# Performance work log

Hardware: AMD Instinct MI355X
Metric: run time of the kernel (lower is better)

The kernel has to match this reference:

```python
import jax, jax.numpy as jnp
import numpy as np

ST_HIDDEN = 128
ST_HEADS = 4
ST_LAYERS = 3
RES_SCALE = 1.0
DK = ST_HIDDEN // ST_HEADS


def build_3d_adj(spatial_ei, spatial_ea, n_nodes, window):
    # replicate spatial edges per time slice with node offset t*n_nodes
    offs = (jnp.arange(window) * n_nodes)[None, :, None]  # [1,W,1]
    all_sp_idx = (spatial_ei[:, None, :] + offs).reshape(2, -1)  # [2, W*E]
    all_sp_attr = jnp.tile(spatial_ea, (window, 1))  # [W*E, De]
    # temporal edges t -> t+1 for every node
    src = jnp.arange((window - 1) * n_nodes)
    temp_idx = jnp.stack([src, src + n_nodes], axis=0)  # [2, (W-1)*N]
    temp_attr = jnp.broadcast_to(spatial_ea.mean(axis=0, keepdims=True),
                                 (temp_idx.shape[1], spatial_ea.shape[1]))
    ei = jnp.concatenate([all_sp_idx, temp_idx], axis=1)
    ea = jnp.concatenate([all_sp_attr, temp_attr], axis=0)
    return ei, ea


def seg_softmax(logits, dst, num_nodes):
    # logits [E,H], segment softmax over dst (pyg_softmax)
    m = jax.ops.segment_max(logits, dst, num_segments=num_nodes)  # [N,H]
    ex = jnp.exp(logits - m[dst])
    s = jax.ops.segment_sum(ex, dst, num_segments=num_nodes)
    return ex / (s[dst] + 1e-16)


def layernorm(x, g, b, eps=1e-5):
    mu = x.mean(-1, keepdims=True)
    var = ((x - mu) ** 2).mean(-1, keepdims=True)
    return (x - mu) * jax.lax.rsqrt(var + eps) * g + b


def block(x, ei, ea, qw, qb, kw, kb, vw, vb, fw, fb, ow, ob, ln_g, ln_b):
    B, Nt, _ = x.shape
    H, dk = ST_HEADS, DK
    Q = (x @ qw + qb).reshape(B, Nt, H, dk)
    K = (x @ kw + kb).reshape(B, Nt, H, dk)
    V = (x @ vw + vb).reshape(B, Nt, H, dk)
    src, dst = ei[0], ei[1]
    q_e = Q[:, dst]  # [B,E,H,dk]
    k_e = K[:, src]
    v_e = V[:, src]
    film = ea @ fw + fb  # [E, 2*hidden]
    gamma, beta = jnp.split(film, 2, axis=-1)
    gamma = gamma.reshape(1, -1, H, dk)
    beta = beta.reshape(1, -1, H, dk)
    k_e = k_e * (1.0 + gamma) + beta
    logits = (q_e * k_e).sum(-1) / np.sqrt(dk).astype(np.float32)  # [B,E,H]
    att = jax.vmap(lambda l: seg_softmax(l, dst, Nt))(logits)
    msg = att[..., None] * v_e  # [B,E,H,dk]
    out = jnp.zeros((B, Nt, H, dk), x.dtype).at[:, dst].add(msg)
    y = out.reshape(B, Nt, H * dk) @ ow + ob
    return layernorm(x + y, ln_g, ln_b)


def setup_inputs() -> dict:
    key = jax.random.key(0)
    ks = jax.random.split(key, 12)
    B, W, N, Fin, E, De = 2, 16, 1000, 16, 16000, 8
    H, L = ST_HIDDEN, ST_LAYERS
    g = lambda k, s: jax.random.normal(k, s, jnp.float32) * 0.05
    return {
        "xw": jax.random.normal(ks[0], (B, W, N, Fin), jnp.float32),
        "spatial_ei": jax.random.randint(ks[1], (2, E), 0, N),
        "spatial_ea": jax.random.normal(ks[2], (E, De), jnp.float32),
        "in_w": g(ks[3], (Fin, H)), "in_b": jnp.zeros((H,), jnp.float32),
        "qw": g(ks[4], (L, H, H)), "qb": jnp.zeros((L, H), jnp.float32),
        "kw": g(ks[5], (L, H, H)), "kb": jnp.zeros((L, H), jnp.float32),
        "vw": g(ks[6], (L, H, H)), "vb": jnp.zeros((L, H), jnp.float32),
        "fw": g(ks[7], (L, De, 2 * H)), "fb": jnp.zeros((L, 2 * H), jnp.float32),
        "ow": g(ks[8], (L, H, H)), "ob": jnp.zeros((L, H), jnp.float32),
        "ln_g": jnp.ones((L, H), jnp.float32), "ln_b": jnp.zeros((L, H), jnp.float32),
        "head_w": g(ks[9], (H, 1)), "head_b": jnp.zeros((1,), jnp.float32),
    }


def reference(xw, spatial_ei, spatial_ea, in_w, in_b, qw, qb, kw, kb, vw, vb,
              fw, fb, ow, ob, ln_g, ln_b, head_w, head_b):
    B, W, N, Fin = xw.shape
    ei, ea = build_3d_adj(spatial_ei, spatial_ea, N, W)
    x = xw.reshape(B, W * N, Fin) @ in_w + in_b
    for l in range(ST_LAYERS):
        bx = block(x, ei, ea, qw[l], qb[l], kw[l], kb[l], vw[l], vb[l],
                   fw[l], fb[l], ow[l], ob[l], ln_g[l], ln_b[l])
        x = x + RES_SCALE * (bx - x)
    last = x.reshape(B, W, N, -1)[:, -1]  # [B,N,H]
    return jax.nn.softplus(last @ head_w + head_b).squeeze(-1)  # [B,N]
```

## Files before the change

kernel.cpp:

```cpp
#include <hip/hip_runtime.h>
#include <math.h>

constexpr int B    = 2;
constexpr int W    = 16;
constexpr int N    = 1000;
constexpr int FIN  = 16;
constexpr int E    = 16000;
constexpr int DE   = 8;
constexpr int H    = 128;
constexpr int L    = 3;
constexpr int WL   = 4;
constexpr int W0G  = 12;
constexpr int RPB  = WL * N;
constexpr int ROWS = B * RPB;

__device__ __forceinline__ float blockSum128(float v) {
  #pragma unroll
  for (int off = 32; off >= 1; off >>= 1) v += __shfl_xor(v, off);
  __shared__ float s2[2];
  int w = threadIdx.x >> 6;
  __syncthreads();
  if ((threadIdx.x & 63) == 0) s2[w] = v;
  __syncthreads();
  return s2[0] + s2[1];
}

__global__ void k_count_scan(const int* __restrict__ ei, int* __restrict__ offs,
                             int* __restrict__ cursor, float* __restrict__ meanea) {
  __shared__ int cnt[N];
  __shared__ int scn[1024];
  int t = threadIdx.x;
  if (t < 8) meanea[t] = 0.f;
  if (t < N) cnt[t] = 0;
  __syncthreads();
  int vals[16];
  int nv = 0;
  for (int e = t; e < E; e += 1024) vals[nv++] = ei[E + e];
  for (int i = 0; i < nv; i++) atomicAdd(&cnt[vals[i]], 1);
  __syncthreads();
  int v = (t < N) ? cnt[t] : 0;
  scn[t] = v;
  __syncthreads();
  for (int st = 1; st < 1024; st <<= 1) {
    int add = (t >= st) ? scn[t - st] : 0;
    __syncthreads();
    scn[t] += add;
    __syncthreads();
  }
  if (t < N) {
    offs[t + 1] = scn[t];
    if (t == 0) offs[0] = 0;
    cursor[t] = scn[t] - v;
  }
}

__global__ void k_prep2(const int* __restrict__ ei, const float* __restrict__ ea,
                        int* __restrict__ cursor, int* __restrict__ csr_src,
                        int* __restrict__ csr_eid, float* __restrict__ meanea) {
  int bid = blockIdx.x;
  int t = threadIdx.x;
  if (bid < 64) {
    int e = bid * 256 + t;
    if (e < E) {
      int src = ei[e];
      int dst = ei[E + e];
      int pos = atomicAdd(&cursor[dst], 1);
      csr_src[pos] = src;
      csr_eid[pos] = e;
    }
  } else {
    __shared__ float sbuf[256];
    int d = t & 7, g = t >> 3;
    float s = 0.f;
    for (int e = (bid - 64) * 32 + g; e < E; e += 64 * 32) s += ea[e * DE + d];
    sbuf[t] = s;
    __syncthreads();
    for (int st = 16; st >= 1; st >>= 1) {
      if (g < st) sbuf[g * 8 + d] += sbuf[(g + st) * 8 + d];
      __syncthreads();
    }
    if (g == 0) atomicAdd(&meanea[d], sbuf[d]);
  }
}

__global__ void k_gemm(const float* __restrict__ X, const float* __restrict__ xw,
                       const float* __restrict__ in_w, const float* __restrict__ in_b,
                       const float* __restrict__ Wq, const float* __restrict__ bq,
                       const float* __restrict__ Wk, const float* __restrict__ bk,
                       const float* __restrict__ Wv, const float* __restrict__ bv,
                       float* __restrict__ Cq, float* __restrict__ Ck, float* __restrict__ Cv,
                       float* __restrict__ xout,
                       int base, int tpb, int fuse_in) {
  int m = blockIdx.y;
  const float* Wm = (m == 0) ? Wq : (m == 1) ? Wk : Wv;
  const float* bm = (m == 0) ? bq : (m == 1) ? bk : bv;
  float* Cm       = (m == 0) ? Cq : (m == 1) ? Ck : Cv;
  int bb = blockIdx.x / tpb;
  int t  = blockIdx.x % tpb;
  int lr0 = base + t * 16;
  int tid = threadIdx.x;
  __shared__ float xs[16][H];
  if (fuse_in) {
    __shared__ float xws[16][FIN];
    for (int i = tid; i < 16 * FIN; i += 128) {
      int rr = i >> 4, k = i & 15;
      int lr = lr0 + rr;
      if (lr < RPB) {
        int wl = lr / N, n = lr % N;
        xws[rr][k] = xw[(((long)bb * W + (W0G + wl)) * N + n) * FIN + k];
      }
    }
    __syncthreads();
    float bc = in_b[tid];
    #pragma unroll
    for (int rr = 0; rr < 16; rr++) {
      float acc = bc;
      #pragma unroll
      for (int k = 0; k < FIN; k++) acc += xws[rr][k] * in_w[k * H + tid];
      xs[rr][tid] = acc;
      int lr = lr0 + rr;
      if (m == 0 && lr < RPB) xout[((long)bb * RPB + lr) * H + tid] = acc;
    }
  } else {
    #pragma unroll
    for (int rr = 0; rr < 16; rr++) {
      int lr = lr0 + rr;
      if (lr < RPB) xs[rr][tid] = X[((long)bb * RPB + lr) * H + tid];
    }
  }
  __syncthreads();
  float bc = bm[tid];
  float acc[16];
  #pragma unroll
  for (int r = 0; r < 16; r++) acc[r] = bc;
  #pragma unroll 4
  for (int k = 0; k < H; k++) {
    float w = Wm[k * H + tid];
    #pragma unroll
    for (int r = 0; r < 16; r++) acc[r] += xs[r][k] * w;
  }
  #pragma unroll
  for (int r = 0; r < 16; r++) {
    int lr = lr0 + r;
    if (lr < RPB) Cm[((long)bb * RPB + lr) * H + tid] = acc[r];
  }
}

__global__ void k_attn_oln(const float* __restrict__ Qb, const float* __restrict__ Kb,
                           const float* __restrict__ Vb,
                           const float* __restrict__ ea, const float* __restrict__ meanea,
                           const float* __restrict__ fw, const float* __restrict__ fb,
                           const int* __restrict__ offs, const int* __restrict__ csr_src,
                           const int* __restrict__ csr_eid,
                           const float* __restrict__ x, const float* __restrict__ ow,
                           const float* __restrict__ ob, const float* __restrict__ lng,
                           const float* __restrict__ lnb, float* __restrict__ xo,
                           int out_lo,
                           const float* __restrict__ hw, const float* __restrict__ hb,
                           float* __restrict__ out, int do_head) {
  __shared__ float fwS[DE][2 * H];
  int tid = threadIdx.x;
  for (int i = tid; i < DE * 2 * H; i += H) fwS[i >> 8][i & 255] = fw[i];

  int nwin = WL - out_lo;
  int idx = blockIdx.x;
  int b = idx / (nwin * N);
  int rem = idx % (nwin * N);
  int wl = out_lo + rem / N;
  int n = rem % N;
  long drow = ((long)b * WL + wl) * N + n;
  float q = Qb[drow * H + tid];
  float fbg = fb[tid], fbb = fb[H + tid];
  long sbase = ((long)b * WL + wl) * N;
  long trow  = ((long)b * WL + wl - 1) * N + n;
  const float scale = 0.17677669529663687f;
  int i0 = offs[n], i1 = offs[n + 1];
  __syncthreads();

  float m = -INFINITY, ssum = 0.f, acc = 0.f;
  for (int base = i0; base <= i1; base += 4) {
    float l[4], vv[4];
    #pragma unroll
    for (int j = 0; j < 4; j++) {
      int i = base + j;
      if (i > i1) { l[j] = -INFINITY; vv[j] = 0.f; continue; }
      long srow; const float* eap; float esc;
      if (i < i1) { srow = sbase + csr_src[i]; eap = ea + (long)csr_eid[i] * DE; esc = 1.f; }
      else        { srow = trow;               eap = meanea;                    esc = 1.f / E; }
      float kv = Kb[srow * H + tid];
      vv[j]    = Vb[srow * H + tid];
      float4 a0 = *(const float4*)(eap);
      float4 a1 = *(const float4*)(eap + 4);
      float a[DE] = {a0.x * esc, a0.y * esc, a0.z * esc, a0.w * esc,
                     a1.x * esc, a1.y * esc, a1.z * esc, a1.w * esc};
      float g = fbg, be = fbb;
      #pragma unroll
      for (int d = 0; d < DE; d++) {
        g  += a[d] * fwS[d][tid];
        be += a[d] * fwS[d][H + tid];
      }
      float p = q * (kv * (1.f + g) + be);
      p += __shfl_xor(p, 16);
      p += __shfl_xor(p, 8);
      p += __shfl_xor(p, 4);
      p += __shfl_xor(p, 2);
      p += __shfl_xor(p, 1);
      l[j] = p * scale;
    }
    float mn = m;
    #pragma unroll
    for (int j = 0; j < 4; j++) mn = fmaxf(mn, l[j]);
    float sc  = __expf(m - mn);
    float pe0 = __expf(l[0] - mn);
    float pe1 = __expf(l[1] - mn);
    float pe2 = __expf(l[2] - mn);
    float pe3 = __expf(l[3] - mn);
    ssum = ssum * sc + ((pe0 + pe1) + (pe2 + pe3));
    acc  = acc  * sc + ((pe0 * vv[0] + pe1 * vv[1]) + (pe2 * vv[2] + pe3 * vv[3]));
    m = mn;
  }
  float ab = acc / (ssum + 1e-16f);

  __shared__ float sab[H];
  sab[tid] = ab;
  __syncthreads();
  float y = ob[tid];
  #pragma unroll 8
  for (int k = 0; k < H; k++) y += sab[k] * ow[k * H + tid];

  float v = x[drow * H + tid] + y;
  float mu = blockSum128(v) * (1.f / H);
  float dv = v - mu;
  float var = blockSum128(dv * dv) * (1.f / H);
  float o = dv * rsqrtf(var + 1e-5f) * lng[tid] + lnb[tid];

  if (!do_head) {
    xo[drow * H + tid] = o;
  } else {
    float hv = o * hw[tid];
    float tot = blockSum128(hv);
    if (tid == 0) {
      float z = tot + hb[0];
      out[b * N + n] = fmaxf(z, 0.f) + log1pf(expf(-fabsf(z)));
    }
  }
}

extern "C" void kernel_launch(void* const* d_in, const int* in_sizes, int n_in,
                              void* d_out, int out_size, void* d_ws, size_t ws_size,
                              hipStream_t stream) {
  const float* xw   = (const float*)d_in[0];
  const int*   ei   = (const int*)d_in[1];
  const float* ea   = (const float*)d_in[2];
  const float* in_w = (const float*)d_in[3];
  const float* in_b = (const float*)d_in[4];
  const float* qw   = (const float*)d_in[5];
  const float* qb   = (const float*)d_in[6];
  const float* kw   = (const float*)d_in[7];
  const float* kb   = (const float*)d_in[8];
  const float* vw   = (const float*)d_in[9];
  const float* vb   = (const float*)d_in[10];
  const float* fw   = (const float*)d_in[11];
  const float* fb   = (const float*)d_in[12];
  const float* ow   = (const float*)d_in[13];
  const float* ob   = (const float*)d_in[14];
  const float* ln_g = (const float*)d_in[15];
  const float* ln_b = (const float*)d_in[16];
  const float* hw   = (const float*)d_in[17];
  const float* hb   = (const float*)d_in[18];
  float* out = (float*)d_out;

  float* ws   = (float*)d_ws;
  float* x    = ws;
  float* x2   = x  + (long)ROWS * H;
  float* Qb   = x2 + (long)ROWS * H;
  float* Kb   = Qb + (long)ROWS * H;
  float* Vb   = Kb + (long)ROWS * H;
  float* meanea  = Vb + (long)ROWS * H;
  int* offs    = (int*)(meanea + 8);
  int* cursor  = offs + N + 1;
  int* csr_src = cursor + N;
  int* csr_eid = csr_src + E;

  k_count_scan<<<1, 1024, 0, stream>>>(ei, offs, cursor, meanea);
  k_prep2<<<128, 256, 0, stream>>>(ei, ea, cursor, csr_src, csr_eid, meanea);

  float* xa = x;
  float* xb = x2;
  for (int l = 0; l < L; l++) {
    int in_lo = l, out_lo = l + 1;
    int rows_pb = (WL - in_lo) * N;
    int tpb = (rows_pb + 15) / 16;
    k_gemm<<<dim3(B * tpb, 3), H, 0, stream>>>(
        xa, xw, in_w, in_b,
        qw + (long)l * H * H, qb + (long)l * H, kw + (long)l * H * H, kb + (long)l * H,
        vw + (long)l * H * H, vb + (long)l * H, Qb, Kb, Vb, xa,
        in_lo * N, tpb, (l == 0) ? 1 : 0);
    int nout = B * (WL - out_lo) * N;
    int last = (l == L - 1) ? 1 : 0;
    k_attn_oln<<<nout, H, 0, stream>>>(
        Qb, Kb, Vb, ea, meanea,
        fw + (long)l * DE * 2 * H, fb + (long)l * 2 * H,
        offs, csr_src, csr_eid,
        xa, ow + (long)l * H * H, ob + (long)l * H,
        ln_g + (long)l * H, ln_b + (long)l * H, xb, out_lo,
        hw, hb, out, last);
    float* tmp = xa; xa = xb; xb = tmp;
  }
}
```

Baseline: 288.8 us.

## Pre-pack weights as float4, retile QKV GEMM, move input projection into prep

Adds a prep stage that repacks all Q/K/V/O weight matrices into a k-grouped float4 layout and computes the input projection there rather than inside the first GEMM. The QKV GEMM now uses 256-thread blocks over 64-row tiles, with each thread holding an 8x4 output register tile and reading weights and activations as float4. The attention kernel keeps the FiLM weights in registers instead of shared memory, drops a barrier, uses DPP for the first two lanes of the head reduction, and reads the packed output weights as float4. The intent is fewer memory transactions and more reuse of each load in the GEMM, at the cost of extra workspace, a larger prep kernel and higher register pressure.

```diff
diff --git a/kernel.cpp b/kernel.cpp
--- a/kernel.cpp
+++ b/kernel.cpp
@@ -13,6 +13,7 @@
 constexpr int W0G  = 12;
 constexpr int RPB  = WL * N;
 constexpr int ROWS = B * RPB;
+constexpr int NMAT = 12;
 
 __device__ __forceinline__ float blockSum128(float v) {
   #pragma unroll
@@ -23,6 +24,26 @@
   if ((threadIdx.x & 63) == 0) s2[w] = v;
   __syncthreads();
   return s2[0] + s2[1];
+}
+
+__device__ __forceinline__ float dpp_add_xor1(float x) {
+  int y = __builtin_amdgcn_update_dpp(0, __float_as_int(x), 0xB1, 0xF, 0xF, true);
+  return x + __int_as_float(y);
+}
+__device__ __forceinline__ float dpp_add_xor2(float x) {
+  int y = __builtin_amdgcn_update_dpp(0, __float_as_int(x), 0x4E, 0xF, 0xF, true);
+  return x + __int_as_float(y);
+}
+__device__ __forceinline__ float headSum32(float p) {
+  p = dpp_add_xor1(p);
+  p = dpp_add_xor2(p);
+  p += __shfl_xor(p, 4);
+  p += __shfl_xor(p, 8);
+  p += __shfl_xor(p, 16);
+  return p;
+}
+__device__ __forceinline__ float dot4(float4 a, float4 b) {
+  return a.x * b.x + a.y * b.y + a.z * b.z + a.w * b.w;
 }
 
 __global__ void k_count_scan(const int* __restrict__ ei, int* __restrict__ offs,
@@ -56,7 +77,12 @@
 
 __global__ void k_prep2(const int* __restrict__ ei, const float* __restrict__ ea,
                         int* __restrict__ cursor, int* __restrict__ csr_src,
-                        int* __restrict__ csr_eid, float* __restrict__ meanea) {
+                        int* __restrict__ csr_eid, float* __restrict__ meanea,
+                        const float* __restrict__ qw, const float* __restrict__ kw,
+                        const float* __restrict__ vw, const float* __restrict__ ow,
+                        float4* __restrict__ wTp4,
+                        const float* __restrict__ xw, const float* __restrict__ in_w,
+                        const float* __restrict__ in_b, float* __restrict__ x) {
   int bid = blockIdx.x;
   int t = threadIdx.x;
   if (bid < 64) {
@@ -68,7 +94,7 @@
       csr_src[pos] = src;
       csr_eid[pos] = e;
     }
-  } else {
+  } else if (bid < 128) {
     __shared__ float sbuf[256];
     int d = t & 7, g = t >> 3;
     float s = 0.f;
@@ -80,69 +106,105 @@
       __syncthreads();
     }
     if (g == 0) atomicAdd(&meanea[d], sbuf[d]);
-  }
-}
-
-__global__ void k_gemm(const float* __restrict__ X, const float* __restrict__ xw,
-                       const float* __restrict__ in_w, const float* __restrict__ in_b,
-                       const float* __restrict__ Wq, const float* __restrict__ bq,
-                       const float* __restrict__ Wk, const float* __restrict__ bk,
-                       const float* __restrict__ Wv, const float* __restrict__ bv,
+  } else if (bid < 128 + NMAT * 16) {
+    int bid2 = bid - 128;
+    int mat = bid2 / 16;
+    int pair = bid2 % 16;
+    int kk4 = pair * 2 + (t >> 7);
+    int c = t & 127;
+    int l = mat >> 2, mm = mat & 3;
+    const float* src = ((mm == 0) ? qw : (mm == 1) ? kw : (mm == 2) ? vw : ow) + (long)l * H * H;
+    int k0 = kk4 * 4;
+    float4 v4;
+    v4.x = src[(k0 + 0) * H + c];
+    v4.y = src[(k0 + 1) * H + c];
+    v4.z = src[(k0 + 2) * H + c];
+    v4.w = src[(k0 + 3) * H + c];
+    wTp4[((long)mat * 32 + kk4) * H + c] = v4;
+  } else {
+    int bi = bid - (128 + NMAT * 16);
+    int b = bi / 63, tt = bi % 63;
+    int lr0 = tt * 64;
+    __shared__ float xwS[64][FIN];
+    __shared__ float inS[FIN][H];
+    for (int i = t; i < 64 * FIN; i += 256) {
+      int r = i >> 4, k = i & 15;
+      int lr = lr0 + r;
+      float val = 0.f;
+      if (lr < RPB) {
+        int wl = lr / N, n = lr % N;
+        val = xw[(((long)b * W + (W0G + wl)) * N + n) * FIN + k];
+      }
+      xwS[r][k] = val;
+    }
+    for (int i = t; i < FIN * H; i += 256) inS[i >> 7][i & 127] = in_w[i];
+    __syncthreads();
+    #pragma unroll
+    for (int qi = 0; qi < 8; qi++) {
+      int idx = t + qi * 256;
+      int r = idx >> 5, cq = idx & 31;
+      int lr = lr0 + r;
+      if (lr < RPB) {
+        float4 acc = *(const float4*)(in_b + cq * 4);
+        #pragma unroll
+        for (int k = 0; k < FIN; k++) {
+          float xv = xwS[r][k];
+          float4 w4 = *(const float4*)(&inS[k][cq * 4]);
+          acc.x += xv * w4.x; acc.y += xv * w4.y; acc.z += xv * w4.z; acc.w += xv * w4.w;
+        }
+        *(float4*)(x + ((long)b * RPB + lr) * H + cq * 4) = acc;
+      }
+    }
+  }
+}
+
+__global__ void k_gemm(const float* __restrict__ X, const float4* __restrict__ wTp4,
+                       int matBase,
+                       const float* __restrict__ bq, const float* __restrict__ bk,
+                       const float* __restrict__ bv,
                        float* __restrict__ Cq, float* __restrict__ Ck, float* __restrict__ Cv,
-                       float* __restrict__ xout,
-                       int base, int tpb, int fuse_in) {
+                       int base, int tiles) {
   int m = blockIdx.y;
-  const float* Wm = (m == 0) ? Wq : (m == 1) ? Wk : Wv;
   const float* bm = (m == 0) ? bq : (m == 1) ? bk : bv;
   float* Cm       = (m == 0) ? Cq : (m == 1) ? Ck : Cv;
-  int bb = blockIdx.x / tpb;
-  int t  = blockIdx.x % tpb;
-  int lr0 = base + t * 16;
-  int tid = threadIdx.x;
-  __shared__ float xs[16][H];
-  if (fuse_in) {
-    __shared__ float xws[16][FIN];
-    for (int i = tid; i < 16 * FIN; i += 128) {
-      int rr = i >> 4, k = i & 15;
-      int lr = lr0 + rr;
-      if (lr < RPB) {
-        int wl = lr / N, n = lr % N;
-        xws[rr][k] = xw[(((long)bb * W + (W0G + wl)) * N + n) * FIN + k];
-      }
-    }
-    __syncthreads();
-    float bc = in_b[tid];
+  const float4* wp = wTp4 + (long)(matBase + m) * 32 * H;
+  int bb = blockIdx.x / tiles;
+  int tt = blockIdx.x % tiles;
+  int lr0 = base + tt * 64;
+  int t = threadIdx.x;
+  int cg = t & 31, rg = t >> 5;
+  __shared__ float xs[64][H];
+  #pragma unroll
+  for (int i = 0; i < 8; i++) {
+    int row = i * 8 + rg;
+    int lr = lr0 + row;
+    float4 v4 = make_float4(0.f, 0.f, 0.f, 0.f);
+    if (lr < RPB) v4 = *(const float4*)(X + ((long)bb * RPB + lr) * H + cg * 4);
+    *(float4*)&xs[row][cg * 4] = v4;
+  }
+  __syncthreads();
+  float4 bias4 = *(const float4*)(bm + cg * 4);
+  float4 acc[8];
+  #pragma unroll
+  for (int i = 0; i < 8; i++) acc[i] = bias4;
+  for (int kk4 = 0; kk4 < 32; kk4++) {
+    float4 w0 = wp[kk4 * H + cg * 4 + 0];
+    float4 w1 = wp[kk4 * H + cg * 4 + 1];
+    float4 w2 = wp[kk4 * H + cg * 4 + 2];
+    float4 w3 = wp[kk4 * H + cg * 4 + 3];
     #pragma unroll
-    for (int rr = 0; rr < 16; rr++) {
-      float acc = bc;
-      #pragma unroll
-      for (int k = 0; k < FIN; k++) acc += xws[rr][k] * in_w[k * H + tid];
-      xs[rr][tid] = acc;
-      int lr = lr0 + rr;
-      if (m == 0 && lr < RPB) xout[((long)bb * RPB + lr) * H + tid] = acc;
-    }
-  } else {
-    #pragma unroll
-    for (int rr = 0; rr < 16; rr++) {
-      int lr = lr0 + rr;
-      if (lr < RPB) xs[rr][tid] = X[((long)bb * RPB + lr) * H + tid];
-    }
-  }
-  __syncthreads();
-  float bc = bm[tid];
-  float acc[16];
-  #pragma unroll
-  for (int r = 0; r < 16; r++) acc[r] = bc;
-  #pragma unroll 4
-  for (int k = 0; k < H; k++) {
-    float w = Wm[k * H + tid];
-    #pragma unroll
-    for (int r = 0; r < 16; r++) acc[r] += xs[r][k] * w;
-  }
-  #pragma unroll
-  for (int r = 0; r < 16; r++) {
-    int lr = lr0 + r;
-    if (lr < RPB) Cm[((long)bb * RPB + lr) * H + tid] = acc[r];
+    for (int i = 0; i < 8; i++) {
+      float4 xv = *(const float4*)&xs[rg * 8 + i][kk4 * 4];
+      acc[i].x += dot4(xv, w0);
+      acc[i].y += dot4(xv, w1);
+      acc[i].z += dot4(xv, w2);
+      acc[i].w += dot4(xv, w3);
+    }
+  }
+  #pragma unroll
+  for (int i = 0; i < 8; i++) {
+    int lr = lr0 + rg * 8 + i;
+    if (lr < RPB) *(float4*)(Cm + ((long)bb * RPB + lr) * H + cg * 4) = acc[i];
   }
 }
 
@@ -152,16 +214,19 @@
                            const float* __restrict__ fw, const float* __restrict__ fb,
                            const int* __restrict__ offs, const int* __restrict__ csr_src,
                            const int* __restrict__ csr_eid,
-                           const float* __restrict__ x, const float* __restrict__ ow,
+                           const float* __restrict__ x, const float4* __restrict__ owp,
                            const float* __restrict__ ob, const float* __restrict__ lng,
                            const float* __restrict__ lnb, float* __restrict__ xo,
                            int out_lo,
                            const float* __restrict__ hw, const float* __restrict__ hb,
                            float* __restrict__ out, int do_head) {
-  __shared__ float fwS[DE][2 * H];
   int tid = threadIdx.x;
-  for (int i = tid; i < DE * 2 * H; i += H) fwS[i >> 8][i & 255] = fw[i];
-
+  float rgw[DE], rbw[DE];
+  #pragma unroll
+  for (int d = 0; d < DE; d++) {
+    rgw[d] = fw[d * 2 * H + tid];
+    rbw[d] = fw[d * 2 * H + H + tid];
+  }
   int nwin = WL - out_lo;
   int idx = blockIdx.x;
   int b = idx / (nwin * N);
@@ -175,7 +240,6 @@
   long trow  = ((long)b * WL + wl - 1) * N + n;
   const float scale = 0.17677669529663687f;
   int i0 = offs[n], i1 = offs[n + 1];
-  __syncthreads();
 
   float m = -INFINITY, ssum = 0.f, acc = 0.f;
   for (int base = i0; base <= i1; base += 4) {
@@ -196,16 +260,11 @@
       float g = fbg, be = fbb;
       #pragma unroll
       for (int d = 0; d < DE; d++) {
-        g  += a[d] * fwS[d][tid];
-        be += a[d] * fwS[d][H + tid];
+        g  += a[d] * rgw[d];
+        be += a[d] * rbw[d];
       }
       float p = q * (kv * (1.f + g) + be);
-      p += __shfl_xor(p, 16);
-      p += __shfl_xor(p, 8);
-      p += __shfl_xor(p, 4);
-      p += __shfl_xor(p, 2);
-      p += __shfl_xor(p, 1);
-      l[j] = p * scale;
+      l[j] = headSum32(p) * scale;
     }
     float mn = m;
     #pragma unroll
@@ -225,8 +284,12 @@
   sab[tid] = ab;
   __syncthreads();
   float y = ob[tid];
-  #pragma unroll 8
-  for (int k = 0; k < H; k++) y += sab[k] * ow[k * H + tid];
+  #pragma unroll 4
+  for (int kk4 = 0; kk4 < 32; kk4++) {
+    float4 w4 = owp[kk4 * H + tid];
+    float4 a4 = *(const float4*)&sab[kk4 * 4];
+    y += dot4(a4, w4);
+  }
 
   float v = x[drow * H + tid] + y;
   float mu = blockSum128(v) * (1.f / H);
@@ -276,33 +339,35 @@
   float* Qb   = x2 + (long)ROWS * H;
   float* Kb   = Qb + (long)ROWS * H;
   float* Vb   = Kb + (long)ROWS * H;
-  float* meanea  = Vb + (long)ROWS * H;
+  float* wTp  = Vb + (long)ROWS * H;
+  float* meanea = wTp + (long)NMAT * H * H;
   int* offs    = (int*)(meanea + 8);
   int* cursor  = offs + N + 1;
   int* csr_src = cursor + N;
   int* csr_eid = csr_src + E;
+  float4* wTp4 = (float4*)wTp;
 
   k_count_scan<<<1, 1024, 0, stream>>>(ei, offs, cursor, meanea);
-  k_prep2<<<128, 256, 0, stream>>>(ei, ea, cursor, csr_src, csr_eid, meanea);
+  k_prep2<<<128 + NMAT * 16 + 126, 256, 0, stream>>>(
+      ei, ea, cursor, csr_src, csr_eid, meanea,
+      qw, kw, vw, ow, wTp4, xw, in_w, in_b, x);
 
   float* xa = x;
   float* xb = x2;
   for (int l = 0; l < L; l++) {
     int in_lo = l, out_lo = l + 1;
     int rows_pb = (WL - in_lo) * N;
-    int tpb = (rows_pb + 15) / 16;
-    k_gemm<<<dim3(B * tpb, 3), H, 0, stream>>>(
-        xa, xw, in_w, in_b,
-        qw + (long)l * H * H, qb + (long)l * H, kw + (long)l * H * H, kb + (long)l * H,
-        vw + (long)l * H * H, vb + (long)l * H, Qb, Kb, Vb, xa,
-        in_lo * N, tpb, (l == 0) ? 1 : 0);
+    int tiles = (rows_pb + 63) / 64;
+    k_gemm<<<dim3(B * tiles, 3), 256, 0, stream>>>(
+        xa, wTp4, l * 4, qb + (long)l * H, kb + (long)l * H, vb + (long)l * H,
+        Qb, Kb, Vb, in_lo * N, tiles);
     int nout = B * (WL - out_lo) * N;
     int last = (l == L - 1) ? 1 : 0;
     k_attn_oln<<<nout, H, 0, stream>>>(
         Qb, Kb, Vb, ea, meanea,
         fw + (long)l * DE * 2 * H, fb + (long)l * 2 * H,
         offs, csr_src, csr_eid,
-        xa, ow + (long)l * H * H, ob + (long)l * H,
+        xa, wTp4 + ((long)l * 4 + 3) * 32 * H, ob + (long)l * H,
         ln_g + (long)l * H, ln_b + (long)l * H, xb, out_lo,
         hw, hb, out, last);
     float* tmp = xa; xa = xb; xb = tmp;
```

After: 293.5 us. No clear change (+1.6%).
